# Performance work log

Hardware: AMD Instinct MI355X
Metric: run time of the kernel (lower is better)

## Reference

```python
import jax, jax.numpy as jnp
import numpy as np

S = 1024   # speakers_per_batch
U = 64     # utterances_per_speaker
D = 256    # embedding_size
EPS = 1e-5


def setup_inputs() -> dict:
    key = jax.random.key(0)
    k1, = jax.random.split(key, 1)
    return {
        "output_of_model": jax.random.normal(k1, (S * U, D), dtype=jnp.float32),
        "similarity_weight": jnp.array([10.0], dtype=jnp.float32),
        "similarity_bias": jnp.array([-5.0], dtype=jnp.float32),
        "speakers_per_batch": S,
        "utterances_per_speaker": U,
    }


def reference(output_of_model, similarity_weight, similarity_bias,
              speakers_per_batch, utterances_per_speaker):
    s, u = speakers_per_batch, utterances_per_speaker
    embeds = output_of_model.reshape(s, u, -1)                      # [S,U,D]

    # inclusive centroids (mean over utterances, L2-normalized with +eps)
    c_incl = jnp.mean(embeds, axis=1)                               # [S,D]
    c_incl = c_incl / (jnp.linalg.norm(c_incl, axis=-1, keepdims=True) + EPS)

    # exclusive centroids (leave-one-out mean, L2-normalized with +eps)
    c_excl = (jnp.sum(embeds, axis=1, keepdims=True) - embeds) / (u - 1)  # [S,U,D]
    c_excl = c_excl / (jnp.linalg.norm(c_excl, axis=-1, keepdims=True) + EPS)

    # normalized embeddings (original normalizes embeds inside the loop)
    e_n = embeds / (jnp.linalg.norm(embeds, axis=-1, keepdims=True) + EPS)

    # off-diagonal: cosine(embed[i,u], incl centroid[j]); diagonal: excl centroid
    sim_incl = jnp.einsum('sud,jd->suj', e_n, c_incl)               # [S,U,S]
    sim_excl = jnp.sum(e_n * c_excl, axis=-1)                       # [S,U]
    diag = jnp.eye(s, dtype=bool)[:, None, :]                       # [S,1,S]
    sim = jnp.where(diag, sim_excl[:, :, None], sim_incl)           # [S,U,S]

    sim = sim * similarity_weight + similarity_bias                 # scaled logits

    logits = sim.reshape(s * u, s)
    targets = jnp.repeat(jnp.arange(s), u)                          # ground truth
    logp = jax.nn.log_softmax(logits, axis=-1)
    loss = -jnp.mean(jnp.take_along_axis(logp, targets[:, None], axis=-1))
    return loss
```

## Files before the change

### kernel.cpp

```cpp
#include <hip/hip_runtime.h>

#define SPK 1024
#define UTT 64
#define DIM 256
#define EPSV 1e-5f
#define NROW (SPK * UTT)
#define NSL 16
#define LOG2E 1.44269504f

typedef __attribute__((ext_vector_type(4))) float f32x4;
typedef __attribute__((ext_vector_type(2))) long long2v;

#define EXP2(x) __builtin_amdgcn_exp2f(x)

__device__ __forceinline__ int pk_fp8(float a, float b, float c, float d) {
    int v = __builtin_amdgcn_cvt_pk_fp8_f32(a, b, 0, false);
    return  __builtin_amdgcn_cvt_pk_fp8_f32(c, d, v, true);
}

__device__ __forceinline__ int fragIdx(int g) {
    return ((g >> 4) * 4 + ((g & 7) >> 1)) * 4 + ((g >> 3) & 1) * 2 + (g & 1);
}

__global__ __launch_bounds__(256, 2)
void k_prep(const float* __restrict__ x,
            unsigned char* __restrict__ cincl8,
            unsigned char* __restrict__ en8,
            float* __restrict__ texcl,
            const float* __restrict__ wp, const float* __restrict__ bp) {
    __shared__ float4 sc4[256];
    __shared__ float4 csq[64];
    __shared__ float sccs;
    int s = blockIdx.x, tid = threadIdx.x;
    int dq = tid & 63, ug = tid >> 6;
    const float4* x4 = (const float4*)(x + (size_t)s * UTT * DIM);

    float4 xv[16];
    float4 p = {0.f, 0.f, 0.f, 0.f};
#pragma unroll
    for (int i = 0; i < 16; ++i) {
        float4 v = x4[(ug * 16 + i) * 64 + dq];
        xv[i] = v;
        p.x += v.x; p.y += v.y; p.z += v.z; p.w += v.w;
    }
    sc4[tid] = p;
    __syncthreads();
    if (tid < 64) {
        float4 a = sc4[dq], b2 = sc4[64 + dq], c = sc4[128 + dq], d = sc4[192 + dq];
        float4 cs = {a.x + b2.x + c.x + d.x, a.y + b2.y + c.y + d.y,
                     a.z + b2.z + c.z + d.z, a.w + b2.w + c.w + d.w};
        csq[dq] = cs;
        float s2 = cs.x * cs.x + cs.y * cs.y + cs.z * cs.z + cs.w * cs.w;
#pragma unroll
        for (int o = 1; o < 64; o <<= 1) s2 += __shfl_xor(s2, o);
        float inv = 16.f / (sqrtf(s2) + UTT * EPSV);
        ((int*)cincl8)[s * 64 + fragIdx(dq)] =
            pk_fp8(cs.x * inv, cs.y * inv, cs.z * inv, cs.w * inv);
        if (tid == 0) sccs = s2;
    }
    __syncthreads();
    float scc = sccs;
    float4 cv = csq[dq];
    float w = wp[0], b = bp[0];

    float sxl[16], scl[16];
#pragma unroll
    for (int i = 0; i < 16; ++i) {
        float4 v = xv[i];
        sxl[i] = v.x * v.x + v.y * v.y + v.z * v.z + v.w * v.w;
        scl[i] = v.x * cv.x + v.y * cv.y + v.z * cv.z + v.w * cv.w;
    }
#pragma unroll
    for (int o = 1; o < 64; o <<= 1)
#pragma unroll
        for (int i = 0; i < 16; ++i) {
            sxl[i] += __shfl_xor(sxl[i], o);
            scl[i] += __shfl_xor(scl[i], o);
        }
    int fi = fragIdx(dq);
#pragma unroll
    for (int i = 0; i < 16; ++i) {
        float inv = 16.f / (sqrtf(sxl[i]) + EPSV);
        ((int*)(en8 + (size_t)(s * UTT + ug * 16 + i) * DIM))[fi] =
            pk_fp8(xv[i].x * inv, xv[i].y * inv, xv[i].z * inv, xv[i].w * inv);
    }
    if (dq == 0) {
#pragma unroll
        for (int i = 0; i < 16; ++i) {
            float nx = sqrtf(sxl[i]);
            float num = scl[i] - sxl[i];
            float e2 = fmaxf(scc - 2.f * scl[i] + sxl[i], 0.f);
            float sim = num / ((nx + EPSV) * (sqrtf(e2) + (UTT - 1) * EPSV));
            texcl[s * UTT + ug * 16 + i] = fmaf(sim, w, b);
        }
    }
}

__global__ __launch_bounds__(256, 4)
void k_main(const unsigned char* __restrict__ en8,
            const unsigned char* __restrict__ cincl8,
            float* __restrict__ partial,
            const float* __restrict__ wp, const float* __restrict__ bp) {
    int tid = threadIdx.x, wave = tid >> 6, lane = tid & 63;
    int quad = lane >> 4, lx = lane & 15;
    int bid = blockIdx.x;
    int g = bid & 3;
    int c = bid >> 2;
    float w = wp[0], b = bp[0];
    float M  = fabsf(w) * 1.0625f + b;
    float wl = w * (LOG2E / 256.f);
    float bl = (b - M) * LOG2E;

    int col0 = g * 256 + wave * 64;
    long2v bf[4][4];
#pragma unroll
    for (int nt = 0; nt < 4; ++nt)
#pragma unroll
        for (int r = 0; r < 4; ++r)
            bf[nt][r] = *(const long2v*)(cincl8 +
                (size_t)(col0 + nt * 16 + lx) * DIM + (r * 4 + quad) * 16);

    for (int sp = 0; sp < 4; ++sp) {
        int s = c * 4 + sp;
        const unsigned char* abase = en8 + (size_t)s * UTT * DIM;
        bool dgw = ((s >> 8) == g) && (((s >> 6) & 3) == wave);
        int nt_d = (s >> 4) & 3, lx_d = s & 15;
        for (int mt = 0; mt < 4; ++mt) {
            long2v af[4];
#pragma unroll
            for (int r = 0; r < 4; ++r)
                af[r] = *(const long2v*)(abase + (mt * 16 + lx) * DIM + (r * 4 + quad) * 16);
            f32x4 acc[4] = {{0.f,0.f,0.f,0.f},{0.f,0.f,0.f,0.f},
                            {0.f,0.f,0.f,0.f},{0.f,0.f,0.f,0.f}};
#pragma unroll
            for (int r = 0; r < 4; ++r) {
#pragma unroll
                for (int nt = 0; nt < 4; ++nt)
                    acc[nt] = __builtin_amdgcn_mfma_f32_16x16x32_fp8_fp8(af[r].x, bf[nt][r].x, acc[nt], 0, 0, 0);
#pragma unroll
                for (int nt = 0; nt < 4; ++nt)
                    acc[nt] = __builtin_amdgcn_mfma_f32_16x16x32_fp8_fp8(af[r].y, bf[nt][r].y, acc[nt], 0, 0, 0);
            }
            float ps[4] = {0.f, 0.f, 0.f, 0.f};
#pragma unroll
            for (int nt = 0; nt < 4; ++nt) {
                bool dgn = dgw && (nt == nt_d);
#pragma unroll
                for (int i = 0; i < 4; ++i) {
                    float e = EXP2(fmaf(acc[nt][i], wl, bl));
                    if (!(dgn && lx == lx_d)) ps[i] += e;
                }
            }
#pragma unroll
            for (int o = 1; o < 16; o <<= 1)
#pragma unroll
                for (int i = 0; i < 4; ++i) ps[i] += __shfl_xor(ps[i], o);
            if (lx == 0)
#pragma unroll
                for (int i = 0; i < 4; ++i)
                    partial[(size_t)(g * 4 + wave) * NROW + (size_t)s * UTT
                            + mt * 16 + quad * 4 + i] = ps[i];
        }
    }
}

__global__ __launch_bounds__(256)
void k_final(const float* __restrict__ partial, const float* __restrict__ texcl,
             const float* __restrict__ wp, const float* __restrict__ bp,
             float* __restrict__ out) {
    int row = blockIdx.x * 256 + threadIdx.x;
    float w = wp[0], b = bp[0];
    float M = fabsf(w) * 1.0625f + b;
    float t = 0.f;
#pragma unroll
    for (int sl = 0; sl < NSL; ++sl) t += partial[(size_t)sl * NROW + row];
    float tex = texcl[row];
    float c = (M + __logf(t + EXP2((tex - M) * LOG2E))) - tex;
#pragma unroll
    for (int o = 1; o < 64; o <<= 1) c += __shfl_xor(c, o);
    __shared__ float red[4];
    if ((threadIdx.x & 63) == 0) red[threadIdx.x >> 6] = c;
    __syncthreads();
    if (threadIdx.x == 0)
        atomicAdd(out, (red[0] + red[1] + red[2] + red[3]) * (1.f / NROW));
}

extern "C" void kernel_launch(void* const* d_in, const int* in_sizes, int n_in,
                              void* d_out, int out_size, void* d_ws, size_t ws_size,
                              hipStream_t stream) {
    const float* x  = (const float*)d_in[0];
    const float* wp = (const float*)d_in[1];
    const float* bp = (const float*)d_in[2];
    char* ws = (char*)d_ws;
    unsigned char* cincl8 = (unsigned char*)ws;
    float* texcl          = (float*)(ws + (1u << 19));
    float* partial        = (float*)(ws + (1u << 20));
    unsigned char* en8    = (unsigned char*)(ws + (8u << 20));
    float* out = (float*)d_out;

    hipMemsetAsync(d_out, 0, sizeof(float), stream);
    k_prep <<<SPK, 256, 0, stream>>>(x, cincl8, en8, texcl, wp, bp);
    k_main <<<4 * (SPK / 4), 256, 0, stream>>>(en8, cincl8, partial, wp, bp);
    k_final<<<NROW / 256, 256, 0, stream>>>(partial, texcl, wp, bp, out);
}
```

Measured before the change: 157.3 us.

## Double-buffer A fragment loads in k_main and halve speakers per block

k_main now prefetches the next A-tile's fp8 fragments into a second register buffer while the current tile's MFMAs run, so global load latency overlaps with compute. The diagonal exclusion is moved out of the hot exp loop into a rare subtract-back path, and partial sums are written as one float4 store. Each block now handles two speakers instead of four, doubling the grid to increase parallelism. An empty asm pins the B fragments in registers. The trade-off is more registers per thread, which could hurt occupancy, and the B fragments are reloaded twice as often in total across blocks.

```diff
diff --git a/kernel.cpp b/kernel.cpp
--- a/kernel.cpp
+++ b/kernel.cpp
@@ -119,49 +119,73 @@
         for (int r = 0; r < 4; ++r)
             bf[nt][r] = *(const long2v*)(cincl8 +
                 (size_t)(col0 + nt * 16 + lx) * DIM + (r * 4 + quad) * 16);
-
-    for (int sp = 0; sp < 4; ++sp) {
-        int s = c * 4 + sp;
+#pragma unroll
+    for (int nt = 0; nt < 4; ++nt)
+#pragma unroll
+        for (int r = 0; r < 4; ++r)
+            asm volatile("" : "+v"(bf[nt][r].x), "+v"(bf[nt][r].y));
+
+    float* pb = partial + (size_t)(g * 4 + wave) * NROW;
+
+#define LOADA(dst, mtv)                                                         \
+    _Pragma("unroll")                                                           \
+    for (int r = 0; r < 4; ++r)                                                 \
+        dst[r] = *(const long2v*)(abase + ((mtv) * 16 + lx) * DIM + (r * 4 + quad) * 16);
+
+#define TILE(afb, mtv) {                                                        \
+    f32x4 acc[4] = {{0.f,0.f,0.f,0.f},{0.f,0.f,0.f,0.f},                        \
+                    {0.f,0.f,0.f,0.f},{0.f,0.f,0.f,0.f}};                       \
+    _Pragma("unroll")                                                           \
+    for (int r = 0; r < 4; ++r) {                                               \
+        _Pragma("unroll")                                                       \
+        for (int nt = 0; nt < 4; ++nt)                                          \
+            acc[nt] = __builtin_amdgcn_mfma_f32_16x16x32_fp8_fp8(afb[r].x, bf[nt][r].x, acc[nt], 0, 0, 0); \
+        _Pragma("unroll")                                                       \
+        for (int nt = 0; nt < 4; ++nt)                                          \
+            acc[nt] = __builtin_amdgcn_mfma_f32_16x16x32_fp8_fp8(afb[r].y, bf[nt][r].y, acc[nt], 0, 0, 0); \
+    }                                                                           \
+    float ps[4] = {0.f, 0.f, 0.f, 0.f};                                         \
+    _Pragma("unroll")                                                           \
+    for (int nt = 0; nt < 4; ++nt)                                              \
+        _Pragma("unroll")                                                       \
+        for (int i = 0; i < 4; ++i)                                             \
+            ps[i] += EXP2(fmaf(acc[nt][i], wl, bl));                            \
+    if (dgw) {                                \
+        _Pragma("unroll")                                                       \
+        for (int nt = 0; nt < 4; ++nt)                                          \
+            if (nt == nt_d)                    \
+                _Pragma("unroll")                                               \
+                for (int i = 0; i < 4; ++i) {                                   \
+                    float e = EXP2(fmaf(acc[nt][i], wl, bl));                   \
+                    if (lx == lx_d) ps[i] -= e;                                 \
+                }                                                               \
+    }                                                                           \
+    _Pragma("unroll")                                                           \
+    for (int o = 1; o < 16; o <<= 1)          \
+        _Pragma("unroll")                                                       \
+        for (int i = 0; i < 4; ++i) ps[i] += __shfl_xor(ps[i], o);              \
+    if (lx == 0)                                                                \
+        *(float4*)(pb + (size_t)s * UTT + (mtv) * 16 + quad * 4) =              \
+            (float4){ps[0], ps[1], ps[2], ps[3]};                               \
+}
+
+    for (int sp = 0; sp < 2; ++sp) {
+        int s = c * 2 + sp;
         const unsigned char* abase = en8 + (size_t)s * UTT * DIM;
         bool dgw = ((s >> 8) == g) && (((s >> 6) & 3) == wave);
         int nt_d = (s >> 4) & 3, lx_d = s & 15;
-        for (int mt = 0; mt < 4; ++mt) {
-            long2v af[4];
-#pragma unroll
-            for (int r = 0; r < 4; ++r)
-                af[r] = *(const long2v*)(abase + (mt * 16 + lx) * DIM + (r * 4 + quad) * 16);
-            f32x4 acc[4] = {{0.f,0.f,0.f,0.f},{0.f,0.f,0.f,0.f},
-                            {0.f,0.f,0.f,0.f},{0.f,0.f,0.f,0.f}};
-#pragma unroll
-            for (int r = 0; r < 4; ++r) {
-#pragma unroll
-                for (int nt = 0; nt < 4; ++nt)
-                    acc[nt] = __builtin_amdgcn_mfma_f32_16x16x32_fp8_fp8(af[r].x, bf[nt][r].x, acc[nt], 0, 0, 0);
-#pragma unroll
-                for (int nt = 0; nt < 4; ++nt)
-                    acc[nt] = __builtin_amdgcn_mfma_f32_16x16x32_fp8_fp8(af[r].y, bf[nt][r].y, acc[nt], 0, 0, 0);
-            }
-            float ps[4] = {0.f, 0.f, 0.f, 0.f};
-#pragma unroll
-            for (int nt = 0; nt < 4; ++nt) {
-                bool dgn = dgw && (nt == nt_d);
-#pragma unroll
-                for (int i = 0; i < 4; ++i) {
-                    float e = EXP2(fmaf(acc[nt][i], wl, bl));
-                    if (!(dgn && lx == lx_d)) ps[i] += e;
-                }
-            }
-#pragma unroll
-            for (int o = 1; o < 16; o <<= 1)
-#pragma unroll
-                for (int i = 0; i < 4; ++i) ps[i] += __shfl_xor(ps[i], o);
-            if (lx == 0)
-#pragma unroll
-                for (int i = 0; i < 4; ++i)
-                    partial[(size_t)(g * 4 + wave) * NROW + (size_t)s * UTT
-                            + mt * 16 + quad * 4 + i] = ps[i];
-        }
-    }
+        long2v afA[4], afB[4];
+        LOADA(afA, 0);
+        LOADA(afB, 1);
+        TILE(afA, 0);
+        LOADA(afA, 2);
+        TILE(afB, 1);
+        LOADA(afB, 3);
+        TILE(afA, 2);
+        TILE(afB, 3);
+    }
+#undef LOADA
+#undef TILE
 }
 
 __global__ __launch_bounds__(256)
@@ -200,6 +224,6 @@
 
     hipMemsetAsync(d_out, 0, sizeof(float), stream);
     k_prep <<<SPK, 256, 0, stream>>>(x, cincl8, en8, texcl, wp, bp);
-    k_main <<<4 * (SPK / 4), 256, 0, stream>>>(en8, cincl8, partial, wp, bp);
+    k_main <<<4 * (SPK / 2), 256, 0, stream>>>(en8, cincl8, partial, wp, bp);
     k_final<<<NROW / 256, 256, 0, stream>>>(partial, texcl, wp, bp, out);
 }
```

Result: slower. 162.3 us (+3.2%).
